# Kernel tuning notes

Measured on AMD Instinct MI355X. Metric: run time of the kernel, lower is better.

## Reference

```python
import jax, jax.numpy as jnp
import numpy as np

N = 50000      # nodes
E = 800000     # edges
D = 128        # node_dim
H = 4          # heads
C = 64         # hidden_dim per head
B = 64         # graphs in batch
OUT = 10       # output_dim
SLOPE = 0.2    # GATConv leaky_relu negative slope (PyG default)


def gat_conv(x, src, dst, W, a_src, a_dst, bias, concat):
    """One PyG-style GATConv layer. src/dst already include self-loops."""
    n = x.shape[0]
    h = (x @ W).reshape(n, H, C)                       # [N,H,C]
    al_s = jnp.sum(h * a_src, axis=-1)                  # [N,H]
    al_d = jnp.sum(h * a_dst, axis=-1)                  # [N,H]
    e = jax.nn.leaky_relu(al_s[src] + al_d[dst], SLOPE)  # [E+N,H]
    m = jax.ops.segment_max(e, dst, num_segments=n)      # per-target-node max
    e = jnp.exp(e - m[dst])
    den = jax.ops.segment_sum(e, dst, num_segments=n)
    alpha = e / (den[dst] + 1e-16)                       # [E+N,H]
    msg = h[src] * alpha[:, :, None]                     # [E+N,H,C]
    out = jax.ops.segment_sum(msg, dst, num_segments=n)  # [N,H,C]
    out = out.reshape(n, H * C) if concat else out.mean(axis=1)
    return out + bias


def gat_forward(x, edge_index, batch, W0, b0, as0, ad0, W1, b1, as1, ad1,
                W2, b2, as2, ad2, pW1, pb1, pW2, pb2):
    n = x.shape[0]
    loop = jnp.arange(n, dtype=edge_index.dtype)
    src = jnp.concatenate([edge_index[0], loop])
    dst = jnp.concatenate([edge_index[1], loop])

    h = gat_conv(x, src, dst, W0, as0, ad0, b0, concat=True)
    h = jax.nn.elu(h)                                    # dropout = identity (eval)
    h = gat_conv(h, src, dst, W1, as1, ad1, b1, concat=True)
    h = jax.nn.elu(h)
    h = gat_conv(h, src, dst, W2, as2, ad2, b2, concat=False)  # [N,C]

    # global_mean_pool
    sums = jax.ops.segment_sum(h, batch, num_segments=B)        # [B,C]
    cnt = jax.ops.segment_sum(jnp.ones((n,), h.dtype), batch, num_segments=B)
    pooled = sums / jnp.maximum(cnt, 1.0)[:, None]

    # predictor MLP
    z = jax.nn.relu(pooled @ pW1 + pb1)
    return z @ pW2 + pb2                                        # [B,OUT]


def setup_inputs() -> dict:
    key = jax.random.key(0)
    ks = jax.random.split(key, 24)
    gl = lambda k, shp, fan: (jax.random.normal(k, shp, jnp.float32) / np.float32(np.sqrt(fan)))
    x = jax.random.normal(ks[0], (N, D), jnp.float32)
    edge_index = jax.random.randint(ks[1], (2, E), 0, N, dtype=jnp.int32)
    batch = jnp.sort(jax.random.randint(ks[2], (N,), 0, B, dtype=jnp.int32))
    return dict(
        x=x, edge_index=edge_index, batch=batch,
        W0=gl(ks[3], (D, H * C), D), b0=jnp.zeros((H * C,), jnp.float32),
        as0=gl(ks[4], (H, C), C), ad0=gl(ks[5], (H, C), C),
        W1=gl(ks[6], (H * C, H * C), H * C), b1=jnp.zeros((H * C,), jnp.float32),
        as1=gl(ks[7], (H, C), C), ad1=gl(ks[8], (H, C), C),
        W2=gl(ks[9], (H * C, H * C), H * C), b2=jnp.zeros((C,), jnp.float32),
        as2=gl(ks[10], (H, C), C), ad2=gl(ks[11], (H, C), C),
        pW1=gl(ks[12], (C, C // 2), C), pb1=jnp.zeros((C // 2,), jnp.float32),
        pW2=gl(ks[13], (C // 2, OUT), C // 2), pb2=jnp.zeros((OUT,), jnp.float32),
    )


def reference(x, edge_index, batch, W0, b0, as0, ad0, W1, b1, as1, ad1,
              W2, b2, as2, ad2, pW1, pb1, pW2, pb2):
    return gat_forward(x, edge_index, batch, W0, b0, as0, ad0, W1, b1, as1, ad1,
                       W2, b2, as2, ad2, pW1, pb1, pW2, pb2)
```

## Files before the change

kernel.cpp:

```cpp
#include <hip/hip_runtime.h>
#include <hip/hip_fp16.h>
#include <cstdint>

#define N_NODES 50000
#define E_EDGES 800000
#define HC 256
#define B_GR 64
#define OUT_DIM 10
#define SLOPE 0.2f
#define NBLK_SCAN ((N_NODES + 255) / 256)

using f16x8 = __attribute__((ext_vector_type(8))) _Float16;
using f32x4 = __attribute__((ext_vector_type(4))) float;

__global__ void wsplit_kernel(const float* __restrict__ W, _Float16* __restrict__ wt_hi,
                              _Float16* __restrict__ wt_lo, int K) {
    int i = blockIdx.x * 256 + threadIdx.x;
    if (i >= K * 256) return;
    int k = i >> 8, n = i & 255;
    float v = W[i];
    _Float16 h = (_Float16)v;
    _Float16 l = (_Float16)(v - (float)h);
    wt_hi[(size_t)n * K + k] = h;
    wt_lo[(size_t)n * K + k] = l;
}

template<int K>
__global__ __launch_bounds__(256) void gemm_mfma(const float* __restrict__ A,
        const _Float16* __restrict__ wt_hi, const _Float16* __restrict__ wt_lo,
        __half* __restrict__ h_half,
        const float* __restrict__ a_src, const float* __restrict__ a_dst,
        float* __restrict__ al_s, float* __restrict__ al_d, int M) {
    __shared__ _Float16 a_hi[64][64];
    __shared__ _Float16 a_lo[64][64];
    int tid = threadIdx.x;
    int w = tid >> 6;
    int l = tid & 63;
    int rr = l & 15;
    int kg = l >> 4;
    int row0 = blockIdx.x * 64;
    int lrow = tid >> 2;
    int lgp  = (tid & 3) * 2;

    f32x4 acc[4][4] = {};

    for (int k0 = 0; k0 < K; k0 += 64) {
        if (k0 > 0) __syncthreads();
        int gr = row0 + lrow;
#pragma unroll
        for (int gi = 0; gi < 2; ++gi) {
            int g = lgp + gi;
            float vv[8];
            if (gr < M) {
                float4 p = *(const float4*)&A[(size_t)gr * K + k0 + g * 8];
                float4 q = *(const float4*)&A[(size_t)gr * K + k0 + g * 8 + 4];
                vv[0] = p.x; vv[1] = p.y; vv[2] = p.z; vv[3] = p.w;
                vv[4] = q.x; vv[5] = q.y; vv[6] = q.z; vv[7] = q.w;
            } else {
#pragma unroll
                for (int j = 0; j < 8; ++j) vv[j] = 0.f;
            }
            f16x8 vh, vl;
#pragma unroll
            for (int j = 0; j < 8; ++j) {
                _Float16 hh = (_Float16)vv[j];
                vh[j] = hh;
                vl[j] = (_Float16)(vv[j] - (float)hh);
            }
            int gs = g ^ (lrow & 7);
            *(f16x8*)&a_hi[lrow][gs * 8] = vh;
            *(f16x8*)&a_lo[lrow][gs * 8] = vl;
        }
        __syncthreads();
#pragma unroll
        for (int c = 0; c < 2; ++c) {
            f16x8 ah[4], alo[4];
#pragma unroll
            for (int fm = 0; fm < 4; ++fm) {
                int row = fm * 16 + rr;
                int gsw = ((c * 4 + kg) ^ (row & 7));
                ah[fm]  = *(const f16x8*)&a_hi[row][gsw * 8];
                alo[fm] = *(const f16x8*)&a_lo[row][gsw * 8];
            }
#pragma unroll
            for (int fn = 0; fn < 4; ++fn) {
                int col = w * 64 + fn * 16 + rr;
                size_t boff = (size_t)col * K + k0 + (c * 4 + kg) * 8;
                f16x8 bh = *(const f16x8*)&wt_hi[boff];
                f16x8 bl = *(const f16x8*)&wt_lo[boff];
#pragma unroll
                for (int fm = 0; fm < 4; ++fm) {
                    acc[fm][fn] = __builtin_amdgcn_mfma_f32_16x16x32_f16(ah[fm],  bh, acc[fm][fn], 0, 0, 0);
                    acc[fm][fn] = __builtin_amdgcn_mfma_f32_16x16x32_f16(ah[fm],  bl, acc[fm][fn], 0, 0, 0);
                    acc[fm][fn] = __builtin_amdgcn_mfma_f32_16x16x32_f16(alo[fm], bh, acc[fm][fn], 0, 0, 0);
                }
            }
        }
    }

    int head = w;
    float asv[4], adv[4];
#pragma unroll
    for (int fn = 0; fn < 4; ++fn) {
        asv[fn] = a_src[head * 64 + fn * 16 + rr];
        adv[fn] = a_dst[head * 64 + fn * 16 + rr];
    }
#pragma unroll
    for (int fm = 0; fm < 4; ++fm) {
#pragma unroll
        for (int r = 0; r < 4; ++r) {
            int row = fm * 16 + kg * 4 + r;
            int gr = row0 + row;
            float ps = acc[fm][0][r] * asv[0] + acc[fm][1][r] * asv[1]
                     + acc[fm][2][r] * asv[2] + acc[fm][3][r] * asv[3];
            float pd = acc[fm][0][r] * adv[0] + acc[fm][1][r] * adv[1]
                     + acc[fm][2][r] * adv[2] + acc[fm][3][r] * adv[3];
#pragma unroll
            for (int off = 1; off < 16; off <<= 1) {
                ps += __shfl_xor(ps, off, 64);
                pd += __shfl_xor(pd, off, 64);
            }
            if (gr < M) {
#pragma unroll
                for (int fn = 0; fn < 4; ++fn)
                    h_half[(size_t)gr * HC + w * 64 + fn * 16 + rr] = __float2half(acc[fm][fn][r]);
                if (rr == 0) {
                    al_s[gr * 4 + head] = ps;
                    al_d[gr * 4 + head] = pd;
                }
            }
        }
    }
}

__global__ void init_cnt(int* cnt) {
    int i = blockIdx.x * blockDim.x + threadIdx.x;
    if (i < N_NODES) cnt[i] = 1;
}
__global__ void hist_kernel(const int* __restrict__ dsts, int* cnt) {
    int i = blockIdx.x * blockDim.x + threadIdx.x;
    if (i < E_EDGES) atomicAdd(&cnt[dsts[i]], 1);
}
__global__ __launch_bounds__(256) void scan_bsum(const int* __restrict__ cnt,
                                                 int* __restrict__ bsum) {
    __shared__ int ws[4];
    int t = threadIdx.x;
    int i = blockIdx.x * 256 + t;
    int v = (i < N_NODES) ? cnt[i] : 0;
#pragma unroll
    for (int off = 1; off < 64; off <<= 1) v += __shfl_xor(v, off, 64);
    if ((t & 63) == 0) ws[t >> 6] = v;
    __syncthreads();
    if (t == 0) bsum[blockIdx.x] = ws[0] + ws[1] + ws[2] + ws[3];
}
__global__ __launch_bounds__(256) void scan_boff(const int* __restrict__ bsum,
                                                 int* __restrict__ boff) {
    __shared__ int s[256];
    int t = threadIdx.x;
    int v = (t < NBLK_SCAN) ? bsum[t] : 0;
    s[t] = v;
    __syncthreads();
    for (int off = 1; off < 256; off <<= 1) {
        int u = (t >= off) ? s[t - off] : 0;
        __syncthreads();
        s[t] += u;
        __syncthreads();
    }
    if (t < NBLK_SCAN) boff[t] = s[t] - v;
}
__global__ __launch_bounds__(256) void scan_final(const int* __restrict__ cnt,
        const int* __restrict__ boff, int* __restrict__ row_ptr,
        int* __restrict__ cursor) {
    __shared__ int s[256];
    int b = blockIdx.x, t = threadIdx.x;
    int i = b * 256 + t;
    int v = (i < N_NODES) ? cnt[i] : 0;
    s[t] = v;
    __syncthreads();
    for (int off = 1; off < 256; off <<= 1) {
        int u = (t >= off) ? s[t - off] : 0;
        __syncthreads();
        s[t] += u;
        __syncthreads();
    }
    int rp = boff[b] + s[t] - v;
    if (i < N_NODES) { row_ptr[i] = rp; cursor[i] = rp; }
    if (i == N_NODES - 1) row_ptr[N_NODES] = rp + v;
}
__global__ void scatter_kernel(const int* __restrict__ srcs, const int* __restrict__ dsts,
                               int* cursor, int* col) {
    int i = blockIdx.x * blockDim.x + threadIdx.x;
    if (i >= E_EDGES + N_NODES) return;
    int s, d;
    if (i < E_EDGES) { s = srcs[i]; d = dsts[i]; }
    else             { s = d = i - E_EDGES; }
    int pos = atomicAdd(&cursor[d], 1);
    col[pos] = s;
}

__global__ __launch_bounds__(256) void agg_kernel(const __half* __restrict__ hh,
        const float* __restrict__ al_s, const float* __restrict__ al_d,
        const int* __restrict__ row_ptr, const int* __restrict__ col,
        const float* __restrict__ bias, float* __restrict__ out, int mode) {
    __shared__ int   lds_col[4][64];
    __shared__ float lds_alpha[4][64 * 4];
    int wid  = threadIdx.x >> 6;
    int node = blockIdx.x * 4 + wid;
    int lane = threadIdx.x & 63;
    if (node >= N_NODES) return;
    int start = row_ptr[node], end = row_ptr[node + 1];
    int deg = end - start;
    const float4 ald = *(const float4*)&al_d[node * 4];
    int head = lane >> 4;
    float ald_h = head == 0 ? ald.x : head == 1 ? ald.y : head == 2 ? ald.z : ald.w;

    float ax = 0.f, ay = 0.f, az = 0.f, aw = 0.f;

    if (deg <= 64) {
        int j = start + lane;
        bool active = j < end;
        int s = active ? col[j] : 0;
        float4 as = *(const float4*)&al_s[s * 4];
        float e0 = as.x + ald.x; e0 = e0 > 0.f ? e0 : SLOPE * e0;
        float e1 = as.y + ald.y; e1 = e1 > 0.f ? e1 : SLOPE * e1;
        float e2 = as.z + ald.z; e2 = e2 > 0.f ? e2 : SLOPE * e2;
        float e3 = as.w + ald.w; e3 = e3 > 0.f ? e3 : SLOPE * e3;
        float m0 = active ? e0 : -1e30f, m1 = active ? e1 : -1e30f;
        float m2 = active ? e2 : -1e30f, m3 = active ? e3 : -1e30f;
#pragma unroll
        for (int off = 1; off < 64; off <<= 1) {
            m0 = fmaxf(m0, __shfl_xor(m0, off, 64));
            m1 = fmaxf(m1, __shfl_xor(m1, off, 64));
            m2 = fmaxf(m2, __shfl_xor(m2, off, 64));
            m3 = fmaxf(m3, __shfl_xor(m3, off, 64));
        }
        float x0 = active ? expf(e0 - m0) : 0.f;
        float x1 = active ? expf(e1 - m1) : 0.f;
        float x2 = active ? expf(e2 - m2) : 0.f;
        float x3 = active ? expf(e3 - m3) : 0.f;
        float d0 = x0, d1 = x1, d2 = x2, d3 = x3;
#pragma unroll
        for (int off = 1; off < 64; off <<= 1) {
            d0 += __shfl_xor(d0, off, 64);
            d1 += __shfl_xor(d1, off, 64);
            d2 += __shfl_xor(d2, off, 64);
            d3 += __shfl_xor(d3, off, 64);
        }
        float4 a4;
        a4.x = x0 / (d0 + 1e-16f); a4.y = x1 / (d1 + 1e-16f);
        a4.z = x2 / (d2 + 1e-16f); a4.w = x3 / (d3 + 1e-16f);
        lds_col[wid][lane] = s;
        *(float4*)&lds_alpha[wid][lane * 4] = a4;
        const int*   lc = lds_col[wid];
        const float* la = lds_alpha[wid];
        for (int t0 = 0; t0 < deg; t0 += 8) {
            int nn = deg - t0;
            float w[8]; float2 raw[8];
#pragma unroll
            for (int k = 0; k < 8; ++k) {
                if (k < nn) {
                    int s2 = lc[t0 + k];
                    w[k] = la[(t0 + k) * 4 + head];
                    raw[k] = *(const float2*)&hh[(size_t)s2 * HC + lane * 4];
                } else {
                    w[k] = 0.f;
                    raw[k] = make_float2(0.f, 0.f);
                }
            }
#pragma unroll
            for (int k = 0; k < 8; ++k) {
                float2 f0 = __half22float2(*(__half2*)&raw[k].x);
                float2 f1 = __half22float2(*(__half2*)&raw[k].y);
                ax = fmaf(w[k], f0.x, ax); ay = fmaf(w[k], f0.y, ay);
                az = fmaf(w[k], f1.x, az); aw = fmaf(w[k], f1.y, aw);
            }
        }
    } else {
        float m0 = -1e30f, m1 = -1e30f, m2 = -1e30f, m3 = -1e30f;
        for (int j = start + lane; j < end; j += 64) {
            int s = col[j];
            float4 as = *(const float4*)&al_s[s * 4];
            float e0 = as.x + ald.x; e0 = e0 > 0.f ? e0 : SLOPE * e0;
            float e1 = as.y + ald.y; e1 = e1 > 0.f ? e1 : SLOPE * e1;
            float e2 = as.z + ald.z; e2 = e2 > 0.f ? e2 : SLOPE * e2;
            float e3 = as.w + ald.w; e3 = e3 > 0.f ? e3 : SLOPE * e3;
            m0 = fmaxf(m0, e0); m1 = fmaxf(m1, e1);
            m2 = fmaxf(m2, e2); m3 = fmaxf(m3, e3);
        }
#pragma unroll
        for (int off = 1; off < 64; off <<= 1) {
            m0 = fmaxf(m0, __shfl_xor(m0, off, 64));
            m1 = fmaxf(m1, __shfl_xor(m1, off, 64));
            m2 = fmaxf(m2, __shfl_xor(m2, off, 64));
            m3 = fmaxf(m3, __shfl_xor(m3, off, 64));
        }
        float d0 = 0.f, d1 = 0.f, d2 = 0.f, d3 = 0.f;
        for (int j = start + lane; j < end; j += 64) {
            int s = col[j];
            float4 as = *(const float4*)&al_s[s * 4];
            float e0 = as.x + ald.x; e0 = e0 > 0.f ? e0 : SLOPE * e0;
            float e1 = as.y + ald.y; e1 = e1 > 0.f ? e1 : SLOPE * e1;
            float e2 = as.z + ald.z; e2 = e2 > 0.f ? e2 : SLOPE * e2;
            float e3 = as.w + ald.w; e3 = e3 > 0.f ? e3 : SLOPE * e3;
            d0 += expf(e0 - m0); d1 += expf(e1 - m1);
            d2 += expf(e2 - m2); d3 += expf(e3 - m3);
        }
#pragma unroll
        for (int off = 1; off < 64; off <<= 1) {
            d0 += __shfl_xor(d0, off, 64);
            d1 += __shfl_xor(d1, off, 64);
            d2 += __shfl_xor(d2, off, 64);
            d3 += __shfl_xor(d3, off, 64);
        }
        float inv0 = 1.f / (d0 + 1e-16f), inv1 = 1.f / (d1 + 1e-16f);
        float inv2 = 1.f / (d2 + 1e-16f), inv3 = 1.f / (d3 + 1e-16f);
        float m_h   = head == 0 ? m0   : head == 1 ? m1   : head == 2 ? m2   : m3;
        float inv_h = head == 0 ? inv0 : head == 1 ? inv1 : head == 2 ? inv2 : inv3;
        for (int jb = start; jb < end; jb += 64) {
            int j = jb + lane;
            int cs = (j < end) ? col[j] : 0;
            int cnt = min(64, end - jb);
            for (int t = 0; t < cnt; ++t) {
                int s = __shfl(cs, t, 64);
                float als = al_s[s * 4 + head];
                float e = als + ald_h; e = e > 0.f ? e : SLOPE * e;
                float w = expf(e - m_h) * inv_h;
                float2 raw = *(const float2*)&hh[(size_t)s * HC + lane * 4];
                float2 f0 = __half22float2(*(__half2*)&raw.x);
                float2 f1 = __half22float2(*(__half2*)&raw.y);
                ax = fmaf(w, f0.x, ax); ay = fmaf(w, f0.y, ay);
                az = fmaf(w, f1.x, az); aw = fmaf(w, f1.y, aw);
            }
        }
    }

    if (mode == 0) {
        float4 b4 = *(const float4*)&bias[lane * 4];
        float vx = ax + b4.x; vx = vx > 0.f ? vx : expm1f(vx);
        float vy = ay + b4.y; vy = vy > 0.f ? vy : expm1f(vy);
        float vz = az + b4.z; vz = vz > 0.f ? vz : expm1f(vz);
        float vw = aw + b4.w; vw = vw > 0.f ? vw : expm1f(vw);
        float4 v = make_float4(vx, vy, vz, vw);
        *(float4*)&out[(size_t)node * HC + lane * 4] = v;
    } else {
#pragma unroll
        for (int off = 16; off < 64; off <<= 1) {
            ax += __shfl_xor(ax, off, 64);
            ay += __shfl_xor(ay, off, 64);
            az += __shfl_xor(az, off, 64);
            aw += __shfl_xor(aw, off, 64);
        }
        if (lane < 16) {
            float4 b4 = *(const float4*)&bias[lane * 4];
            float4 v = make_float4(ax * 0.25f + b4.x, ay * 0.25f + b4.y,
                                   az * 0.25f + b4.z, aw * 0.25f + b4.w);
            *(float4*)&out[(size_t)node * 64 + lane * 4] = v;
        }
    }
}

__global__ void pool_zero(float* __restrict__ pooled) {
    int i = blockIdx.x * blockDim.x + threadIdx.x;
    if (i < B_GR * 64) pooled[i] = 0.f;
}

__global__ __launch_bounds__(256) void pool_kernel(const float* __restrict__ act,
        const int* __restrict__ batch, float* __restrict__ pooled) {
    int b = blockIdx.x;
    int chunk = blockIdx.y;
    int warp = threadIdx.x >> 6;
    int lane = threadIdx.x & 63;
    int lo = 0, hi = N_NODES;
    while (lo < hi) { int mid = (lo + hi) >> 1; if (batch[mid] < b) lo = mid + 1; else hi = mid; }
    int s = lo;
    lo = 0; hi = N_NODES;
    while (lo < hi) { int mid = (lo + hi) >> 1; if (batch[mid] < b + 1) lo = mid + 1; else hi = mid; }
    int e = lo;
    float sum = 0.f;
    for (int n = s + chunk * 4 + warp; n < e; n += 64)
        sum += act[(size_t)n * 64 + lane];
    atomicAdd(&pooled[b * 64 + lane], sum);
}

__global__ __launch_bounds__(64) void mlp_kernel(const float* __restrict__ pooled,
        const int* __restrict__ batch,
        const float* __restrict__ pW1, const float* __restrict__ pb1,
        const float* __restrict__ pW2, const float* __restrict__ pb2,
        float* __restrict__ outp) {
    __shared__ float p[64];
    __shared__ float z[32];
    int b = blockIdx.x, t = threadIdx.x;
    int lo = 0, hi = N_NODES;
    while (lo < hi) { int mid = (lo + hi) >> 1; if (batch[mid] < b) lo = mid + 1; else hi = mid; }
    int s = lo;
    lo = 0; hi = N_NODES;
    while (lo < hi) { int mid = (lo + hi) >> 1; if (batch[mid] < b + 1) lo = mid + 1; else hi = mid; }
    int e = lo;
    float inv = 1.f / (float)max(e - s, 1);
    p[t] = pooled[b * 64 + t] * inv;
    __syncthreads();
    if (t < 32) {
        float s2 = pb1[t];
        for (int c = 0; c < 64; ++c) s2 += p[c] * pW1[c * 32 + t];
        z[t] = s2 > 0.f ? s2 : 0.f;
    }
    __syncthreads();
    if (t < OUT_DIM) {
        float s2 = pb2[t];
        for (int k = 0; k < 32; ++k) s2 += z[k] * pW2[k * 10 + t];
        outp[b * 10 + t] = s2;
    }
}

extern "C" void kernel_launch(void* const* d_in, const int* in_sizes, int n_in,
                              void* d_out, int out_size, void* d_ws, size_t ws_size,
                              hipStream_t stream) {
    const float* x    = (const float*)d_in[0];
    const int*   ei   = (const int*)d_in[1];
    const int*   batch= (const int*)d_in[2];
    const float* W0   = (const float*)d_in[3];
    const float* b0   = (const float*)d_in[4];
    const float* as0  = (const float*)d_in[5];
    const float* ad0  = (const float*)d_in[6];
    const float* W1   = (const float*)d_in[7];
    const float* b1   = (const float*)d_in[8];
    const float* as1  = (const float*)d_in[9];
    const float* ad1  = (const float*)d_in[10];
    const float* W2   = (const float*)d_in[11];
    const float* b2   = (const float*)d_in[12];
    const float* as2  = (const float*)d_in[13];
    const float* ad2  = (const float*)d_in[14];
    const float* pW1  = (const float*)d_in[15];
    const float* pb1  = (const float*)d_in[16];
    const float* pW2  = (const float*)d_in[17];
    const float* pb2  = (const float*)d_in[18];
    float* out = (float*)d_out;

    char* ws = (char*)d_ws;
    size_t off = 0;
    auto alloc = [&](size_t bytes) -> void* {
        void* p = ws + off;
        off += (bytes + 255) & ~(size_t)255;
        return p;
    };
    __half* h_half = (__half*)alloc((size_t)N_NODES * HC * 2);
    float* act    = (float*)alloc((size_t)N_NODES * HC * 4);
    float* als    = (float*)alloc((size_t)N_NODES * 4 * 4);
    float* ald    = (float*)alloc((size_t)N_NODES * 4 * 4);
    int*   cnt    = (int*)alloc((size_t)N_NODES * 4);
    int*   row_ptr= (int*)alloc((size_t)(N_NODES + 1) * 4);
    int*   cursor = (int*)alloc((size_t)N_NODES * 4);
    int*   col    = (int*)alloc((size_t)(E_EDGES + N_NODES) * 4);
    float* pooled = (float*)alloc((size_t)B_GR * 64 * 4);
    int*   bsum   = (int*)alloc((size_t)NBLK_SCAN * 4);
    int*   boff   = (int*)alloc((size_t)NBLK_SCAN * 4);
    _Float16* w0h = (_Float16*)alloc((size_t)128 * 256 * 2);
    _Float16* w0l = (_Float16*)alloc((size_t)128 * 256 * 2);
    _Float16* w1h = (_Float16*)alloc((size_t)256 * 256 * 2);
    _Float16* w1l = (_Float16*)alloc((size_t)256 * 256 * 2);
    _Float16* w2h = (_Float16*)alloc((size_t)256 * 256 * 2);
    _Float16* w2l = (_Float16*)alloc((size_t)256 * 256 * 2);

    const int* srcs = ei;
    const int* dsts = ei + E_EDGES;

    wsplit_kernel<<<(128 * 256 + 255) / 256, 256, 0, stream>>>(W0, w0h, w0l, 128);
    wsplit_kernel<<<(256 * 256 + 255) / 256, 256, 0, stream>>>(W1, w1h, w1l, 256);
    wsplit_kernel<<<(256 * 256 + 255) / 256, 256, 0, stream>>>(W2, w2h, w2l, 256);

    init_cnt<<<(N_NODES + 255) / 256, 256, 0, stream>>>(cnt);
    hist_kernel<<<(E_EDGES + 255) / 256, 256, 0, stream>>>(dsts, cnt);
    scan_bsum<<<NBLK_SCAN, 256, 0, stream>>>(cnt, bsum);
    scan_boff<<<1, 256, 0, stream>>>(bsum, boff);
    scan_final<<<NBLK_SCAN, 256, 0, stream>>>(cnt, boff, row_ptr, cursor);
    scatter_kernel<<<(E_EDGES + N_NODES + 255) / 256, 256, 0, stream>>>(srcs, dsts, cursor, col);

    int gblk = (N_NODES + 63) / 64;
    int nblk = (N_NODES + 3) / 4;

    gemm_mfma<128><<<gblk, 256, 0, stream>>>(x, w0h, w0l, h_half, as0, ad0, als, ald, N_NODES);
    agg_kernel<<<nblk, 256, 0, stream>>>(h_half, als, ald, row_ptr, col, b0, act, 0);
    gemm_mfma<256><<<gblk, 256, 0, stream>>>(act, w1h, w1l, h_half, as1, ad1, als, ald, N_NODES);
    agg_kernel<<<nblk, 256, 0, stream>>>(h_half, als, ald, row_ptr, col, b1, act, 0);
    gemm_mfma<256><<<gblk, 256, 0, stream>>>(act, w2h, w2l, h_half, as2, ad2, als, ald, N_NODES);
    agg_kernel<<<nblk, 256, 0, stream>>>(h_half, als, ald, row_ptr, col, b2, act, 1);

    pool_zero<<<(B_GR * 64 + 255) / 256, 256, 0, stream>>>(pooled);
    dim3 pgrid(B_GR, 16);
    pool_kernel<<<pgrid, 256, 0, stream>>>(act, batch, pooled);
    mlp_kernel<<<B_GR, 64, 0, stream>>>(pooled, batch, pW1, pb1, pW2, pb2, out);
}
```

Before: 461.7 us.

## Pack two nodes per wavefront in aggregation and tile weight layout for GEMM

The aggregation kernel now gives each 64-lane wavefront two destination nodes, 32 lanes each, when both degrees are at most 32. Each lane loads 8 halfs (16 bytes) per neighbor, which halves the shuffle-reduction width and puts more nodes in flight per wave. Higher-degree pairs fall back to the old per-node path, run sequentially over the two nodes. The weight-split kernel also writes the fp16 hi/lo weights in a K-chunked layout so the GEMM's B-fragment loads are contiguous. N_NODES is divisible by 8, so the nodeB bounds check is dropped.

```diff
diff --git a/kernel.cpp b/kernel.cpp
--- a/kernel.cpp
+++ b/kernel.cpp
@@ -21,8 +21,9 @@
     float v = W[i];
     _Float16 h = (_Float16)v;
     _Float16 l = (_Float16)(v - (float)h);
-    wt_hi[(size_t)n * K + k] = h;
-    wt_lo[(size_t)n * K + k] = l;
+    int oidx = ((((k >> 5) * 256 + n) * 4) + ((k >> 3) & 3)) * 8 + (k & 7);
+    wt_hi[oidx] = h;
+    wt_lo[oidx] = l;
 }
 
 template<int K>
@@ -82,10 +83,11 @@
                 ah[fm]  = *(const f16x8*)&a_hi[row][gsw * 8];
                 alo[fm] = *(const f16x8*)&a_lo[row][gsw * 8];
             }
+            int chunk = (k0 >> 5) + c;
 #pragma unroll
             for (int fn = 0; fn < 4; ++fn) {
                 int col = w * 64 + fn * 16 + rr;
-                size_t boff = (size_t)col * K + k0 + (c * 4 + kg) * 8;
+                size_t boff = (((size_t)chunk * 256 + col) * 4 + kg) * 8;
                 f16x8 bh = *(const f16x8*)&wt_hi[boff];
                 f16x8 bl = *(const f16x8*)&wt_lo[boff];
 #pragma unroll
@@ -203,23 +205,25 @@
         const int* __restrict__ row_ptr, const int* __restrict__ col,
         const float* __restrict__ bias, float* __restrict__ out, int mode) {
     __shared__ int   lds_col[4][64];
-    __shared__ float lds_alpha[4][64 * 4];
+    __shared__ float lds_alpha[4][64][4];
     int wid  = threadIdx.x >> 6;
-    int node = blockIdx.x * 4 + wid;
     int lane = threadIdx.x & 63;
-    if (node >= N_NODES) return;
-    int start = row_ptr[node], end = row_ptr[node + 1];
-    int deg = end - start;
-    const float4 ald = *(const float4*)&al_d[node * 4];
-    int head = lane >> 4;
-    float ald_h = head == 0 ? ald.x : head == 1 ? ald.y : head == 2 ? ald.z : ald.w;
-
-    float ax = 0.f, ay = 0.f, az = 0.f, aw = 0.f;
-
-    if (deg <= 64) {
-        int j = start + lane;
-        bool active = j < end;
-        int s = active ? col[j] : 0;
+    int hf   = lane >> 5;
+    int ln   = lane & 31;
+    int nodeA = blockIdx.x * 8 + wid * 2;
+    int nodeB = nodeA + 1;
+    int sA = row_ptr[nodeA], eA = row_ptr[nodeA + 1];
+    int sB = row_ptr[nodeB], eB = row_ptr[nodeB + 1];
+    int degA = eA - sA, degB = eB - sB;
+
+    if (degA <= 32 && degB <= 32) {
+        int node  = hf ? nodeB : nodeA;
+        int start = hf ? sB : sA;
+        int deg   = hf ? degB : degA;
+        int degmax = max(degA, degB);
+        const float4 ald = *(const float4*)&al_d[node * 4];
+        bool active = ln < deg;
+        int s = active ? col[start + ln] : 0;
         float4 as = *(const float4*)&al_s[s * 4];
         float e0 = as.x + ald.x; e0 = e0 > 0.f ? e0 : SLOPE * e0;
         float e1 = as.y + ald.y; e1 = e1 > 0.f ? e1 : SLOPE * e1;
@@ -228,7 +232,7 @@
         float m0 = active ? e0 : -1e30f, m1 = active ? e1 : -1e30f;
         float m2 = active ? e2 : -1e30f, m3 = active ? e3 : -1e30f;
 #pragma unroll
-        for (int off = 1; off < 64; off <<= 1) {
+        for (int off = 1; off < 32; off <<= 1) {
             m0 = fmaxf(m0, __shfl_xor(m0, off, 64));
             m1 = fmaxf(m1, __shfl_xor(m1, off, 64));
             m2 = fmaxf(m2, __shfl_xor(m2, off, 64));
@@ -240,7 +244,7 @@
         float x3 = active ? expf(e3 - m3) : 0.f;
         float d0 = x0, d1 = x1, d2 = x2, d3 = x3;
 #pragma unroll
-        for (int off = 1; off < 64; off <<= 1) {
+        for (int off = 1; off < 32; off <<= 1) {
             d0 += __shfl_xor(d0, off, 64);
             d1 += __shfl_xor(d1, off, 64);
             d2 += __shfl_xor(d2, off, 64);
@@ -249,112 +253,213 @@
         float4 a4;
         a4.x = x0 / (d0 + 1e-16f); a4.y = x1 / (d1 + 1e-16f);
         a4.z = x2 / (d2 + 1e-16f); a4.w = x3 / (d3 + 1e-16f);
-        lds_col[wid][lane] = s;
-        *(float4*)&lds_alpha[wid][lane * 4] = a4;
-        const int*   lc = lds_col[wid];
-        const float* la = lds_alpha[wid];
-        for (int t0 = 0; t0 < deg; t0 += 8) {
-            int nn = deg - t0;
-            float w[8]; float2 raw[8];
-#pragma unroll
-            for (int k = 0; k < 8; ++k) {
-                if (k < nn) {
-                    int s2 = lc[t0 + k];
-                    w[k] = la[(t0 + k) * 4 + head];
-                    raw[k] = *(const float2*)&hh[(size_t)s2 * HC + lane * 4];
-                } else {
-                    w[k] = 0.f;
-                    raw[k] = make_float2(0.f, 0.f);
-                }
-            }
-#pragma unroll
-            for (int k = 0; k < 8; ++k) {
-                float2 f0 = __half22float2(*(__half2*)&raw[k].x);
-                float2 f1 = __half22float2(*(__half2*)&raw[k].y);
-                ax = fmaf(w[k], f0.x, ax); ay = fmaf(w[k], f0.y, ay);
-                az = fmaf(w[k], f1.x, az); aw = fmaf(w[k], f1.y, aw);
-            }
-        }
-    } else {
-        float m0 = -1e30f, m1 = -1e30f, m2 = -1e30f, m3 = -1e30f;
-        for (int j = start + lane; j < end; j += 64) {
-            int s = col[j];
+        int e = hf * 32 + ln;
+        lds_col[wid][e] = s;
+        *(float4*)&lds_alpha[wid][e][0] = a4;
+        int head = ln >> 3;
+        int ch0 = ln * 8;
+        float acc[8] = {0.f, 0.f, 0.f, 0.f, 0.f, 0.f, 0.f, 0.f};
+        int ebase = hf * 32;
+        for (int t0 = 0; t0 < degmax; t0 += 4) {
+            float wv[4]; float4 raw[4];
+#pragma unroll
+            for (int k = 0; k < 4; ++k) {
+                int t = t0 + k;
+                int tt = min(t, deg - 1);
+                int s2 = lds_col[wid][ebase + tt];
+                wv[k] = (t < deg) ? lds_alpha[wid][ebase + tt][head] : 0.f;
+                raw[k] = *(const float4*)&hh[(size_t)s2 * HC + ch0];
+            }
+#pragma unroll
+            for (int k = 0; k < 4; ++k) {
+                const __half2* hp = (const __half2*)&raw[k];
+                float2 f0 = __half22float2(hp[0]);
+                float2 f1 = __half22float2(hp[1]);
+                float2 f2 = __half22float2(hp[2]);
+                float2 f3 = __half22float2(hp[3]);
+                acc[0] = fmaf(wv[k], f0.x, acc[0]); acc[1] = fmaf(wv[k], f0.y, acc[1]);
+                acc[2] = fmaf(wv[k], f1.x, acc[2]); acc[3] = fmaf(wv[k], f1.y, acc[3]);
+                acc[4] = fmaf(wv[k], f2.x, acc[4]); acc[5] = fmaf(wv[k], f2.y, acc[5]);
+                acc[6] = fmaf(wv[k], f3.x, acc[6]); acc[7] = fmaf(wv[k], f3.y, acc[7]);
+            }
+        }
+        if (mode == 0) {
+            float b8[8];
+            *(float4*)&b8[0] = *(const float4*)&bias[ch0];
+            *(float4*)&b8[4] = *(const float4*)&bias[ch0 + 4];
+            float v[8];
+#pragma unroll
+            for (int j = 0; j < 8; ++j) {
+                float t = acc[j] + b8[j];
+                v[j] = t > 0.f ? t : expm1f(t);
+            }
+            *(float4*)&out[(size_t)node * HC + ch0]     = *(float4*)&v[0];
+            *(float4*)&out[(size_t)node * HC + ch0 + 4] = *(float4*)&v[4];
+        } else {
+#pragma unroll
+            for (int j = 0; j < 8; ++j) {
+                acc[j] += __shfl_xor(acc[j], 8, 64);
+                acc[j] += __shfl_xor(acc[j], 16, 64);
+            }
+            if (ln < 8) {
+                float v[8];
+#pragma unroll
+                for (int j = 0; j < 8; ++j)
+                    v[j] = acc[j] * 0.25f + bias[ln * 8 + j];
+                *(float4*)&out[(size_t)node * 64 + ln * 8]     = *(float4*)&v[0];
+                *(float4*)&out[(size_t)node * 64 + ln * 8 + 4] = *(float4*)&v[4];
+            }
+        }
+        return;
+    }
+
+    for (int nn = 0; nn < 2; ++nn) {
+        int node = nodeA + nn;
+        int start = row_ptr[node], end = row_ptr[node + 1];
+        int deg = end - start;
+        const float4 ald = *(const float4*)&al_d[node * 4];
+        int head = lane >> 4;
+        float ald_h = head == 0 ? ald.x : head == 1 ? ald.y : head == 2 ? ald.z : ald.w;
+        float ax = 0.f, ay = 0.f, az = 0.f, aw = 0.f;
+
+        if (deg <= 64) {
+            int j = start + lane;
+            bool active = j < end;
+            int s = active ? col[j] : 0;
             float4 as = *(const float4*)&al_s[s * 4];
             float e0 = as.x + ald.x; e0 = e0 > 0.f ? e0 : SLOPE * e0;
             float e1 = as.y + ald.y; e1 = e1 > 0.f ? e1 : SLOPE * e1;
             float e2 = as.z + ald.z; e2 = e2 > 0.f ? e2 : SLOPE * e2;
             float e3 = as.w + ald.w; e3 = e3 > 0.f ? e3 : SLOPE * e3;
-            m0 = fmaxf(m0, e0); m1 = fmaxf(m1, e1);
-            m2 = fmaxf(m2, e2); m3 = fmaxf(m3, e3);
-        }
-#pragma unroll
-        for (int off = 1; off < 64; off <<= 1) {
-            m0 = fmaxf(m0, __shfl_xor(m0, off, 64));
-            m1 = fmaxf(m1, __shfl_xor(m1, off, 64));
-            m2 = fmaxf(m2, __shfl_xor(m2, off, 64));
-            m3 = fmaxf(m3, __shfl_xor(m3, off, 64));
-        }
-        float d0 = 0.f, d1 = 0.f, d2 = 0.f, d3 = 0.f;
-        for (int j = start + lane; j < end; j += 64) {
-            int s = col[j];
-            float4 as = *(const float4*)&al_s[s * 4];
-            float e0 = as.x + ald.x; e0 = e0 > 0.f ? e0 : SLOPE * e0;
-            float e1 = as.y + ald.y; e1 = e1 > 0.f ? e1 : SLOPE * e1;
-            float e2 = as.z + ald.z; e2 = e2 > 0.f ? e2 : SLOPE * e2;
-            float e3 = as.w + ald.w; e3 = e3 > 0.f ? e3 : SLOPE * e3;
-            d0 += expf(e0 - m0); d1 += expf(e1 - m1);
-            d2 += expf(e2 - m2); d3 += expf(e3 - m3);
-        }
-#pragma unroll
-        for (int off = 1; off < 64; off <<= 1) {
-            d0 += __shfl_xor(d0, off, 64);
-            d1 += __shfl_xor(d1, off, 64);
-            d2 += __shfl_xor(d2, off, 64);
-            d3 += __shfl_xor(d3, off, 64);
-        }
-        float inv0 = 1.f / (d0 + 1e-16f), inv1 = 1.f / (d1 + 1e-16f);
-        float inv2 = 1.f / (d2 + 1e-16f), inv3 = 1.f / (d3 + 1e-16f);
-        float m_h   = head == 0 ? m0   : head == 1 ? m1   : head == 2 ? m2   : m3;
-        float inv_h = head == 0 ? inv0 : head == 1 ? inv1 : head == 2 ? inv2 : inv3;
-        for (int jb = start; jb < end; jb += 64) {
-            int j = jb + lane;
-            int cs = (j < end) ? col[j] : 0;
-            int cnt = min(64, end - jb);
-            for (int t = 0; t < cnt; ++t) {
-                int s = __shfl(cs, t, 64);
-                float als = al_s[s * 4 + head];
-                float e = als + ald_h; e = e > 0.f ? e : SLOPE * e;
-                float w = expf(e - m_h) * inv_h;
-                float2 raw = *(const float2*)&hh[(size_t)s * HC + lane * 4];
-                float2 f0 = __half22float2(*(__half2*)&raw.x);
-                float2 f1 = __half22float2(*(__half2*)&raw.y);
-                ax = fmaf(w, f0.x, ax); ay = fmaf(w, f0.y, ay);
-                az = fmaf(w, f1.x, az); aw = fmaf(w, f1.y, aw);
-            }
-        }
-    }
-
-    if (mode == 0) {
-        float4 b4 = *(const float4*)&bias[lane * 4];
-        float vx = ax + b4.x; vx = vx > 0.f ? vx : expm1f(vx);
-        float vy = ay + b4.y; vy = vy > 0.f ? vy : expm1f(vy);
-        float vz = az + b4.z; vz = vz > 0.f ? vz : expm1f(vz);
-        float vw = aw + b4.w; vw = vw > 0.f ? vw : expm1f(vw);
-        float4 v = make_float4(vx, vy, vz, vw);
-        *(float4*)&out[(size_t)node * HC + lane * 4] = v;
-    } else {
-#pragma unroll
-        for (int off = 16; off < 64; off <<= 1) {
-            ax += __shfl_xor(ax, off, 64);
-            ay += __shfl_xor(ay, off, 64);
-            az += __shfl_xor(az, off, 64);
-            aw += __shfl_xor(aw, off, 64);
-        }
-        if (lane < 16) {
+            float m0 = active ? e0 : -1e30f, m1 = active ? e1 : -1e30f;
+            float m2 = active ? e2 : -1e30f, m3 = active ? e3 : -1e30f;
+#pragma unroll
+            for (int off = 1; off < 64; off <<= 1) {
+                m0 = fmaxf(m0, __shfl_xor(m0, off, 64));
+                m1 = fmaxf(m1, __shfl_xor(m1, off, 64));
+                m2 = fmaxf(m2, __shfl_xor(m2, off, 64));
+                m3 = fmaxf(m3, __shfl_xor(m3, off, 64));
+            }
+            float x0 = active ? expf(e0 - m0) : 0.f;
+            float x1 = active ? expf(e1 - m1) : 0.f;
+            float x2 = active ? expf(e2 - m2) : 0.f;
+            float x3 = active ? expf(e3 - m3) : 0.f;
+            float d0 = x0, d1 = x1, d2 = x2, d3 = x3;
+#pragma unroll
+            for (int off = 1; off < 64; off <<= 1) {
+                d0 += __shfl_xor(d0, off, 64);
+                d1 += __shfl_xor(d1, off, 64);
+                d2 += __shfl_xor(d2, off, 64);
+                d3 += __shfl_xor(d3, off, 64);
+            }
+            float4 a4;
+            a4.x = x0 / (d0 + 1e-16f); a4.y = x1 / (d1 + 1e-16f);
+            a4.z = x2 / (d2 + 1e-16f); a4.w = x3 / (d3 + 1e-16f);
+            lds_col[wid][lane] = s;
+            *(float4*)&lds_alpha[wid][lane][0] = a4;
+            for (int t0 = 0; t0 < deg; t0 += 8) {
+                int nr = deg - t0;
+                float wv[8]; float2 raw[8];
+#pragma unroll
+                for (int k = 0; k < 8; ++k) {
+                    if (k < nr) {
+                        int s2 = lds_col[wid][t0 + k];
+                        wv[k] = lds_alpha[wid][t0 + k][head];
+                        raw[k] = *(const float2*)&hh[(size_t)s2 * HC + lane * 4];
+                    } else {
+                        wv[k] = 0.f;
+                        raw[k] = make_float2(0.f, 0.f);
+                    }
+                }
+#pragma unroll
+                for (int k = 0; k < 8; ++k) {
+                    float2 f0 = __half22float2(*(__half2*)&raw[k].x);
+                    float2 f1 = __half22float2(*(__half2*)&raw[k].y);
+                    ax = fmaf(wv[k], f0.x, ax); ay = fmaf(wv[k], f0.y, ay);
+                    az = fmaf(wv[k], f1.x, az); aw = fmaf(wv[k], f1.y, aw);
+                }
+            }
+        } else {
+            float m0 = -1e30f, m1 = -1e30f, m2 = -1e30f, m3 = -1e30f;
+            for (int j = start + lane; j < end; j += 64) {
+                int s = col[j];
+                float4 as = *(const float4*)&al_s[s * 4];
+                float e0 = as.x + ald.x; e0 = e0 > 0.f ? e0 : SLOPE * e0;
+                float e1 = as.y + ald.y; e1 = e1 > 0.f ? e1 : SLOPE * e1;
+                float e2 = as.z + ald.z; e2 = e2 > 0.f ? e2 : SLOPE * e2;
+                float e3 = as.w + ald.w; e3 = e3 > 0.f ? e3 : SLOPE * e3;
+                m0 = fmaxf(m0, e0); m1 = fmaxf(m1, e1);
+                m2 = fmaxf(m2, e2); m3 = fmaxf(m3, e3);
+            }
+#pragma unroll
+            for (int off = 1; off < 64; off <<= 1) {
+                m0 = fmaxf(m0, __shfl_xor(m0, off, 64));
+                m1 = fmaxf(m1, __shfl_xor(m1, off, 64));
+                m2 = fmaxf(m2, __shfl_xor(m2, off, 64));
+                m3 = fmaxf(m3, __shfl_xor(m3, off, 64));
+            }
+            float d0 = 0.f, d1 = 0.f, d2 = 0.f, d3 = 0.f;
+            for (int j = start + lane; j < end; j += 64) {
+                int s = col[j];
+                float4 as = *(const float4*)&al_s[s * 4];
+                float e0 = as.x + ald.x; e0 = e0 > 0.f ? e0 : SLOPE * e0;
+                float e1 = as.y + ald.y; e1 = e1 > 0.f ? e1 : SLOPE * e1;
+                float e2 = as.z + ald.z; e2 = e2 > 0.f ? e2 : SLOPE * e2;
+                float e3 = as.w + ald.w; e3 = e3 > 0.f ? e3 : SLOPE * e3;
+                d0 += expf(e0 - m0); d1 += expf(e1 - m1);
+                d2 += expf(e2 - m2); d3 += expf(e3 - m3);
+            }
+#pragma unroll
+            for (int off = 1; off < 64; off <<= 1) {
+                d0 += __shfl_xor(d0, off, 64);
+                d1 += __shfl_xor(d1, off, 64);
+                d2 += __shfl_xor(d2, off, 64);
+                d3 += __shfl_xor(d3, off, 64);
+            }
+            float inv0 = 1.f / (d0 + 1e-16f), inv1 = 1.f / (d1 + 1e-16f);
+            float inv2 = 1.f / (d2 + 1e-16f), inv3 = 1.f / (d3 + 1e-16f);
+            float m_h   = head == 0 ? m0   : head == 1 ? m1   : head == 2 ? m2   : m3;
+            float inv_h = head == 0 ? inv0 : head == 1 ? inv1 : head == 2 ? inv2 : inv3;
+            for (int jb = start; jb < end; jb += 64) {
+                int j = jb + lane;
+                int cs = (j < end) ? col[j] : 0;
+                int cnt2 = min(64, end - jb);
+                for (int t = 0; t < cnt2; ++t) {
+                    int s = __shfl(cs, t, 64);
+                    float als2 = al_s[s * 4 + head];
+                    float e = als2 + ald_h; e = e > 0.f ? e : SLOPE * e;
+                    float wv = expf(e - m_h) * inv_h;
+                    float2 raw = *(const float2*)&hh[(size_t)s * HC + lane * 4];
+                    float2 f0 = __half22float2(*(__half2*)&raw.x);
+                    float2 f1 = __half22float2(*(__half2*)&raw.y);
+                    ax = fmaf(wv, f0.x, ax); ay = fmaf(wv, f0.y, ay);
+                    az = fmaf(wv, f1.x, az); aw = fmaf(wv, f1.y, aw);
+                }
+            }
+        }
+
+        if (mode == 0) {
             float4 b4 = *(const float4*)&bias[lane * 4];
-            float4 v = make_float4(ax * 0.25f + b4.x, ay * 0.25f + b4.y,
-                                   az * 0.25f + b4.z, aw * 0.25f + b4.w);
-            *(float4*)&out[(size_t)node * 64 + lane * 4] = v;
+            float vx = ax + b4.x; vx = vx > 0.f ? vx : expm1f(vx);
+            float vy = ay + b4.y; vy = vy > 0.f ? vy : expm1f(vy);
+            float vz = az + b4.z; vz = vz > 0.f ? vz : expm1f(vz);
+            float vw = aw + b4.w; vw = vw > 0.f ? vw : expm1f(vw);
+            float4 v = make_float4(vx, vy, vz, vw);
+            *(float4*)&out[(size_t)node * HC + lane * 4] = v;
+        } else {
+#pragma unroll
+            for (int off = 16; off < 64; off <<= 1) {
+                ax += __shfl_xor(ax, off, 64);
+                ay += __shfl_xor(ay, off, 64);
+                az += __shfl_xor(az, off, 64);
+                aw += __shfl_xor(aw, off, 64);
+            }
+            if (lane < 16) {
+                float4 b4 = *(const float4*)&bias[lane * 4];
+                float4 v = make_float4(ax * 0.25f + b4.x, ay * 0.25f + b4.y,
+                                       az * 0.25f + b4.z, aw * 0.25f + b4.w);
+                *(float4*)&out[(size_t)node * 64 + lane * 4] = v;
+            }
         }
     }
 }
@@ -476,7 +581,7 @@
     scatter_kernel<<<(E_EDGES + N_NODES + 255) / 256, 256, 0, stream>>>(srcs, dsts, cursor, col);
 
     int gblk = (N_NODES + 63) / 64;
-    int nblk = (N_NODES + 3) / 4;
+    int nblk = (N_NODES + 7) / 8;
 
     gemm_mfma<128><<<gblk, 256, 0, stream>>>(x, w0h, w0l, h_half, as0, ad0, als, ald, N_NODES);
     agg_kernel<<<nblk, 256, 0, stream>>>(h_half, als, ald, row_ptr, col, b0, act, 0);
```

After: 445.0 us. 3.6% less time.
